# Performance work log

Hardware: AMD Instinct MI355X
Metric: run time of the kernel (lower is better)

## Reference

```python
import jax, jax.numpy as jnp
import numpy as np

HIDDEN = 1024
NUM_HEADS = 16
HEAD_DIM = HIDDEN // NUM_HEADS


def setup_inputs() -> dict:
    key = jax.random.key(0)
    ks = jax.random.split(key, 10)
    B, S = 2, 2048
    inp = {
        "hidden_state": jax.random.normal(ks[0], (B, S, HIDDEN), dtype=jnp.float32),
        "attention_mask": jnp.ones((B, S), dtype=jnp.int32),
        # Linear params (weights stored as [in, out] for x @ W + b)
        "Wq": jax.random.normal(ks[1], (HIDDEN, HIDDEN), dtype=jnp.float32) * 0.02,
        "bq": jnp.zeros((HIDDEN,), dtype=jnp.float32),
        "Wk": jax.random.normal(ks[2], (HIDDEN, HEAD_DIM), dtype=jnp.float32) * 0.02,
        "bk": jnp.zeros((HEAD_DIM,), dtype=jnp.float32),
        "Wv": jax.random.normal(ks[3], (HIDDEN, HEAD_DIM), dtype=jnp.float32) * 0.02,
        "bv": jnp.zeros((HEAD_DIM,), dtype=jnp.float32),
        "Wo": jax.random.normal(ks[4], (HIDDEN, HIDDEN), dtype=jnp.float32) * 0.02,
        "bo": jnp.zeros((HIDDEN,), dtype=jnp.float32),
    }
    return inp


def reference(hidden_state, attention_mask, Wq, bq, Wk, bk, Wv, bv, Wo, bo):
    B, S, H = hidden_state.shape
    nH, hd = NUM_HEADS, HEAD_DIM
    q = hidden_state @ Wq + bq                      # [B,S,H]
    k = hidden_state @ Wk + bk                      # [B,S,hd] (single shared KV head)
    v = hidden_state @ Wv + bv                      # [B,S,hd]
    q = q.reshape(B, S, nH, hd).transpose(0, 2, 1, 3)  # [B,nH,S,hd]
    # scores: broadcast shared K across heads
    scores = jnp.einsum("bhqd,bkd->bhqk", q, k) / jnp.sqrt(jnp.float32(hd))
    mask = (attention_mask[:, None, None, :] != 0)
    scores = jnp.where(mask, scores, jnp.float32(-jnp.inf))
    attn = jax.nn.softmax(scores, axis=-1)          # [B,nH,S,S]
    ctx = jnp.einsum("bhqk,bkd->bhqd", attn, v)     # [B,nH,S,hd]
    ctx = ctx.transpose(0, 2, 1, 3).reshape(B, S, H)
    return ctx @ Wo + bo
```

## Files before the change

kernel.cpp:

```cpp
#include <hip/hip_runtime.h>

#define SEQ   2048
#define NHEAD 16
#define HD    64
#define HID   1024
#define NQKV  1152
#define MROWS 4096

typedef unsigned short u16;
typedef unsigned int u32;
typedef __attribute__((ext_vector_type(8))) __bf16 bfrag;
typedef __attribute__((ext_vector_type(4))) float f32x4;
typedef __attribute__((ext_vector_type(4))) short s16x4;

__device__ __forceinline__ u16 f2bf(float f) {
  unsigned u = __float_as_uint(f);
  u += 0x7fffu + ((u >> 16) & 1u);
  return (u16)(u >> 16);
}

__global__ void k_cvt_x(const float* __restrict__ x, u16* __restrict__ o) {
  int i = (blockIdx.x * 256 + threadIdx.x) * 4;
  float4 v = *reinterpret_cast<const float4*>(x + i);
  s16x4 r;
  r.x = (short)f2bf(v.x); r.y = (short)f2bf(v.y);
  r.z = (short)f2bf(v.z); r.w = (short)f2bf(v.w);
  *reinterpret_cast<s16x4*>(o + i) = r;
}

__global__ void k_tr(const float* __restrict__ src, int ld, u16* __restrict__ dst, int nOff) {
  __shared__ float T[64][65];
  const int t = threadIdx.x;
  const int k0 = blockIdx.x * 64, n0 = blockIdx.y * 64;
#pragma unroll
  for (int p = 0; p < 4; ++p) {
    int r = p * 16 + (t >> 4), c = (t & 15) * 4;
    float4 v = *reinterpret_cast<const float4*>(&src[(size_t)(k0 + r) * ld + n0 + c]);
    T[r][c] = v.x; T[r][c + 1] = v.y; T[r][c + 2] = v.z; T[r][c + 3] = v.w;
  }
  __syncthreads();
#pragma unroll
  for (int p = 0; p < 2; ++p) {
    int cc = t + p * 256;
    int n = cc >> 3, k8 = (cc & 7) * 8;
    union { float4 v; u16 u[8]; } o;
#pragma unroll
    for (int j = 0; j < 8; ++j) o.u[j] = f2bf(T[k8 + j][n]);
    *reinterpret_cast<float4*>(&dst[(size_t)(nOff + n0 + n) * 1024 + k0 + k8]) = o.v;
  }
}

__global__ void k_bias(const float* __restrict__ bq, const float* __restrict__ bk,
                       const float* __restrict__ bv, float* __restrict__ bqkv) {
  int t = blockIdx.x * 256 + threadIdx.x;
  if (t >= NQKV) return;
  float v;
  if (t < 1024)      v = bq[t];
  else if (t < 1088) v = bk[t - 1024];
  else               v = bv[t - 1088];
  bqkv[t] = v;
}

__global__ void k_mb(const int* __restrict__ am, float* __restrict__ Mbias) {
  int t = blockIdx.x * 256 + threadIdx.x;
  if (t < 2 * SEQ) Mbias[t] = am[t] ? 0.0f : -1e30f;
}

__global__ void k_vt(const u16* __restrict__ QKV, u16* __restrict__ Vt) {
  int t = blockIdx.x * 256 + threadIdx.x;
  int s = t & 2047, d = (t >> 11) & 63, b = t >> 17;
  Vt[t] = QKV[(size_t)(b * SEQ + s) * NQKV + 1088 + d];
}

template <int STORE_BF16>
__global__ __launch_bounds__(256) void k_gemm(const u16* __restrict__ A,
                                              const u16* __restrict__ Bt,
                                              const float* __restrict__ bias,
                                              void* __restrict__ Cout,
                                              int M, int N, int K) {
  __shared__ __align__(16) u16 Al[128 * 64];
  __shared__ __align__(16) u16 Bl[64 * 64];
  const int tid = threadIdx.x;
  const int lane = tid & 63, l16 = lane & 15, lg = lane >> 4;
  const int wid = tid >> 6;
  const int m0 = blockIdx.x * 128, n0 = blockIdx.y * 64;
  f32x4 acc[2][4] = {};
  for (int k0 = 0; k0 < K; k0 += 64) {
#pragma unroll
    for (int p = 0; p < 4; ++p) {
      int c = tid + p * 256;
      int r = c >> 3, sl = c & 7;
      __builtin_amdgcn_global_load_lds(
          (__attribute__((address_space(1))) void*)(A + (size_t)(m0 + r) * K + k0 + ((sl ^ (r & 7)) << 3)),
          (__attribute__((address_space(3))) void*)(Al + c * 8), 16, 0, 0);
    }
#pragma unroll
    for (int p = 0; p < 2; ++p) {
      int c = tid + p * 256;
      int r = c >> 3, sl = c & 7;
      __builtin_amdgcn_global_load_lds(
          (__attribute__((address_space(1))) void*)(Bt + (size_t)(n0 + r) * K + k0 + ((sl ^ (r & 7)) << 3)),
          (__attribute__((address_space(3))) void*)(Bl + c * 8), 16, 0, 0);
    }
    __syncthreads();
#pragma unroll
    for (int kk = 0; kk < 2; ++kk) {
      bfrag a[2], b[4];
#pragma unroll
      for (int mi = 0; mi < 2; ++mi) {
        int row = wid * 32 + mi * 16 + l16;
        a[mi] = *reinterpret_cast<const bfrag*>(
            Al + row * 64 + ((((kk << 2) | lg) ^ (l16 & 7)) << 3));
      }
#pragma unroll
      for (int ni = 0; ni < 4; ++ni) {
        int row = ni * 16 + l16;
        b[ni] = *reinterpret_cast<const bfrag*>(
            Bl + row * 64 + ((((kk << 2) | lg) ^ (l16 & 7)) << 3));
      }
#pragma unroll
      for (int mi = 0; mi < 2; ++mi)
#pragma unroll
        for (int ni = 0; ni < 4; ++ni)
          acc[mi][ni] = __builtin_amdgcn_mfma_f32_16x16x32_bf16(a[mi], b[ni], acc[mi][ni], 0, 0, 0);
    }
    __syncthreads();
  }
#pragma unroll
  for (int mi = 0; mi < 2; ++mi)
#pragma unroll
    for (int ni = 0; ni < 4; ++ni) {
      int col = n0 + ni * 16 + l16;
      float bb = bias[col];
#pragma unroll
      for (int r = 0; r < 4; ++r) {
        int row = m0 + wid * 32 + mi * 16 + lg * 4 + r;
        float v = acc[mi][ni][r] + bb;
        if (STORE_BF16) ((u16*)Cout)[(size_t)row * N + col] = f2bf(v);
        else            ((float*)Cout)[(size_t)row * N + col] = v;
      }
    }
}

__global__ __launch_bounds__(256, 4) void k_attn(const u16* __restrict__ QKV,
                                                 const u16* __restrict__ Vt,
                                                 const float* __restrict__ Mbias,
                                                 u16* __restrict__ ctx) {
  __shared__ __align__(16) u16 Kl[2][64 * 64];
  __shared__ __align__(16) u16 Pl[4][16][72];
  const int tid = threadIdx.x;
  const int lane = tid & 63, l16 = lane & 15, lg = lane >> 4, wid = tid >> 6;
  const int q0 = blockIdx.x * 64 + wid * 16;
  const int h = blockIdx.y, b = blockIdx.z;

  const u16* Qrow = QKV + (size_t)(b * SEQ + q0 + l16) * NQKV + h * 64;
  const bfrag aq0 = *reinterpret_cast<const bfrag*>(Qrow + lg * 8);
  const bfrag aq1 = *reinterpret_cast<const bfrag*>(Qrow + 32 + lg * 8);
  const u16* Vb = Vt + (size_t)b * 64 * SEQ;
  const u16* Kg = QKV + (size_t)b * SEQ * NQKV + HID;
  const float* mb = Mbias + b * SEQ;

  auto stage_k = [&](int buf, int kv) {
#pragma unroll
    for (int hh = 0; hh < 2; ++hh) {
      int c = tid + hh * 256;
      int r = c >> 3, cb = (c & 7) ^ (r & 7);
      __builtin_amdgcn_global_load_lds(
          (__attribute__((address_space(1))) void*)(Kg + (size_t)(kv + r) * NQKV + cb * 8),
          (__attribute__((address_space(3))) void*)(&Kl[buf][c * 8]), 16, 0, 0);
    }
  };

  stage_k(0, 0);
  __syncthreads();

  float mrun = -1e30f, lrun = 0.0f;
  f32x4 accO[4] = {};

  for (int it = 0; it < SEQ / 64; ++it) {
    const int kv = it * 64;
    const int cur = it & 1;
    if (it + 1 < SEQ / 64) stage_k(cur ^ 1, kv + 64);

    bfrag vf[4][2];
#pragma unroll
    for (int nt = 0; nt < 4; ++nt)
#pragma unroll
      for (int kb = 0; kb < 2; ++kb)
        vf[nt][kb] = *reinterpret_cast<const bfrag*>(
            Vb + (size_t)(nt * 16 + l16) * SEQ + kv + kb * 32 + lg * 8);

    f32x4 s[4];
#pragma unroll
    for (int nt = 0; nt < 4; ++nt) {
      f32x4 z = {};
      {
        int row = nt * 16 + l16;
        int cb0 = (0 * 4 + lg) ^ (l16 & 7);
        int cb1 = (1 * 4 + lg) ^ (l16 & 7);
        bfrag ak0 = *reinterpret_cast<const bfrag*>(&Kl[cur][row * 64 + cb0 * 8]);
        bfrag ak1 = *reinterpret_cast<const bfrag*>(&Kl[cur][row * 64 + cb1 * 8]);
        z = __builtin_amdgcn_mfma_f32_16x16x32_bf16(ak0, aq0, z, 0, 0, 0);
        z = __builtin_amdgcn_mfma_f32_16x16x32_bf16(ak1, aq1, z, 0, 0, 0);
      }
      s[nt] = z;
    }
#pragma unroll
    for (int nt = 0; nt < 4; ++nt) {
      f32x4 mbv = *reinterpret_cast<const f32x4*>(&mb[kv + nt * 16 + lg * 4]);
#pragma unroll
      for (int r = 0; r < 4; ++r)
        s[nt][r] = s[nt][r] * 0.125f + mbv[r];
    }
    float tmax = s[0][0];
#pragma unroll
    for (int nt = 0; nt < 4; ++nt)
#pragma unroll
      for (int r = 0; r < 4; ++r) tmax = fmaxf(tmax, s[nt][r]);
    tmax = fmaxf(tmax, __shfl_xor(tmax, 16));
    tmax = fmaxf(tmax, __shfl_xor(tmax, 32));
    float mnew = fmaxf(mrun, tmax);
    float alpha = __expf(mrun - mnew);
    mrun = mnew;
    float rsum = 0.0f;
#pragma unroll
    for (int nt = 0; nt < 4; ++nt)
#pragma unroll
      for (int r = 0; r < 4; ++r) {
        s[nt][r] = __expf(s[nt][r] - mnew);
        rsum += s[nt][r];
      }
    rsum += __shfl_xor(rsum, 16);
    rsum += __shfl_xor(rsum, 32);
    lrun = lrun * alpha + rsum;
    float ar[4];
#pragma unroll
    for (int r = 0; r < 4; ++r) ar[r] = __shfl(alpha, lg * 4 + r);
#pragma unroll
    for (int nt = 0; nt < 4; ++nt)
#pragma unroll
      for (int r = 0; r < 4; ++r) accO[nt][r] *= ar[r];
#pragma unroll
    for (int nt = 0; nt < 4; ++nt)
#pragma unroll
      for (int r = 0; r < 4; ++r)
        Pl[wid][l16][nt * 16 + lg * 4 + r] = f2bf(s[nt][r]);
    bfrag ap0 = *reinterpret_cast<const bfrag*>(&Pl[wid][l16][lg * 8]);
    bfrag ap1 = *reinterpret_cast<const bfrag*>(&Pl[wid][l16][32 + lg * 8]);
#pragma unroll
    for (int nt = 0; nt < 4; ++nt) {
      accO[nt] = __builtin_amdgcn_mfma_f32_16x16x32_bf16(ap0, vf[nt][0], accO[nt], 0, 0, 0);
      accO[nt] = __builtin_amdgcn_mfma_f32_16x16x32_bf16(ap1, vf[nt][1], accO[nt], 0, 0, 0);
    }
    __syncthreads();
  }

  float linv = 1.0f / lrun;
  float lr[4];
#pragma unroll
  for (int r = 0; r < 4; ++r) lr[r] = __shfl(linv, lg * 4 + r);
#pragma unroll
  for (int nt = 0; nt < 4; ++nt)
#pragma unroll
    for (int r = 0; r < 4; ++r)
      ctx[(size_t)(b * SEQ + q0 + lg * 4 + r) * HID + h * 64 + nt * 16 + l16] =
          f2bf(accO[nt][r] * lr[r]);
}

extern "C" void kernel_launch(void* const* d_in, const int* in_sizes, int n_in,
                              void* d_out, int out_size, void* d_ws, size_t ws_size,
                              hipStream_t stream) {
  const float* x  = (const float*)d_in[0];
  const int* am   = (const int*)d_in[1];
  const float* Wq = (const float*)d_in[2];
  const float* bq = (const float*)d_in[3];
  const float* Wk = (const float*)d_in[4];
  const float* bk = (const float*)d_in[5];
  const float* Wv = (const float*)d_in[6];
  const float* bv = (const float*)d_in[7];
  const float* Wo = (const float*)d_in[8];
  const float* bo = (const float*)d_in[9];

  char* ws = (char*)d_ws;
  u16*  Xb     = (u16*)(ws + 0);
  u16*  Wt_qkv = (u16*)(ws + 8388608);
  u16*  Wt_o   = (u16*)(ws + 10747904);
  float* bqkv  = (float*)(ws + 12845056);
  float* Mbias = (float*)(ws + 12849664);
  u16*  QKV    = (u16*)(ws + 12866048);
  u16*  Vt     = (u16*)(ws + 22303232);
  u16*  ctx    = (u16*)(ws + 22827520);

  k_cvt_x<<<4096, 256, 0, stream>>>(x, Xb);
  k_tr<<<dim3(16, 16), 256, 0, stream>>>(Wq, 1024, Wt_qkv, 0);
  k_tr<<<dim3(16, 1), 256, 0, stream>>>(Wk, 64, Wt_qkv, 1024);
  k_tr<<<dim3(16, 1), 256, 0, stream>>>(Wv, 64, Wt_qkv, 1088);
  k_tr<<<dim3(16, 16), 256, 0, stream>>>(Wo, 1024, Wt_o, 0);
  k_bias<<<5, 256, 0, stream>>>(bq, bk, bv, bqkv);
  k_mb<<<16, 256, 0, stream>>>(am, Mbias);

  dim3 g1(32, 18);
  k_gemm<1><<<g1, 256, 0, stream>>>(Xb, Wt_qkv, bqkv, (void*)QKV, MROWS, NQKV, HID);

  k_vt<<<1024, 256, 0, stream>>>(QKV, Vt);

  dim3 g2(SEQ / 64, NHEAD, 2);
  k_attn<<<g2, 256, 0, stream>>>(QKV, Vt, Mbias, ctx);

  dim3 g3(32, 16);
  k_gemm<0><<<g3, 256, 0, stream>>>(ctx, Wt_o, bo, d_out, MROWS, HID, HID);
}
```

Before: 278.5 us.

## Rework attention with 32x32 MFMA, lazy rescaling and tiled V transpose

Result: faster. 225.2 us (-19.1%).

```diff
diff --git a/kernel.cpp b/kernel.cpp
--- a/kernel.cpp
+++ b/kernel.cpp
@@ -11,12 +11,19 @@
 typedef unsigned int u32;
 typedef __attribute__((ext_vector_type(8))) __bf16 bfrag;
 typedef __attribute__((ext_vector_type(4))) float f32x4;
+typedef __attribute__((ext_vector_type(16))) float f32x16;
 typedef __attribute__((ext_vector_type(4))) short s16x4;
 
 __device__ __forceinline__ u16 f2bf(float f) {
   unsigned u = __float_as_uint(f);
   u += 0x7fffu + ((u >> 16) & 1u);
   return (u16)(u >> 16);
+}
+
+__device__ __forceinline__ u32 cvtpk_bf16(float lo, float hi) {
+  u32 r;
+  asm("v_cvt_pk_bf16_f32 %0, %1, %2" : "=v"(r) : "v"(lo), "v"(hi));
+  return r;
 }
 
 __global__ void k_cvt_x(const float* __restrict__ x, u16* __restrict__ o) {
@@ -67,9 +74,26 @@
 }
 
 __global__ void k_vt(const u16* __restrict__ QKV, u16* __restrict__ Vt) {
-  int t = blockIdx.x * 256 + threadIdx.x;
-  int s = t & 2047, d = (t >> 11) & 63, b = t >> 17;
-  Vt[t] = QKV[(size_t)(b * SEQ + s) * NQKV + 1088 + d];
+  __shared__ u16 T[64][72];
+  const int t = threadIdx.x;
+  const int s0 = blockIdx.x * 64, b = blockIdx.y;
+#pragma unroll
+  for (int p = 0; p < 2; ++p) {
+    int c = t + p * 256;
+    int r = c >> 3, ch = c & 7;
+    *reinterpret_cast<float4*>(&T[r][ch * 8]) = *reinterpret_cast<const float4*>(
+        &QKV[(size_t)(b * SEQ + s0 + r) * NQKV + 1088 + ch * 8]);
+  }
+  __syncthreads();
+#pragma unroll
+  for (int p = 0; p < 2; ++p) {
+    int cc = t + p * 256;
+    int d = cc >> 3, sc = cc & 7;
+    union { float4 v; u16 u[8]; } o;
+#pragma unroll
+    for (int j = 0; j < 8; ++j) o.u[j] = T[sc * 8 + j][d];
+    *reinterpret_cast<float4*>(&Vt[((size_t)b * 64 + d) * SEQ + s0 + sc * 8]) = o.v;
+  }
 }
 
 template <int STORE_BF16>
@@ -142,28 +166,31 @@
     }
 }
 
-__global__ __launch_bounds__(256, 4) void k_attn(const u16* __restrict__ QKV,
+__global__ __launch_bounds__(128, 2) void k_attn(const u16* __restrict__ QKV,
                                                  const u16* __restrict__ Vt,
                                                  const float* __restrict__ Mbias,
                                                  u16* __restrict__ ctx) {
   __shared__ __align__(16) u16 Kl[2][64 * 64];
-  __shared__ __align__(16) u16 Pl[4][16][72];
+  __shared__ __align__(16) u16 Pl[2][32][72];
   const int tid = threadIdx.x;
-  const int lane = tid & 63, l16 = lane & 15, lg = lane >> 4, wid = tid >> 6;
-  const int q0 = blockIdx.x * 64 + wid * 16;
+  const int lane = tid & 63, l32 = lane & 31, hi = lane >> 5, wid = tid >> 6;
+  const int qw = blockIdx.x * 64 + wid * 32;
   const int h = blockIdx.y, b = blockIdx.z;
 
-  const u16* Qrow = QKV + (size_t)(b * SEQ + q0 + l16) * NQKV + h * 64;
-  const bfrag aq0 = *reinterpret_cast<const bfrag*>(Qrow + lg * 8);
-  const bfrag aq1 = *reinterpret_cast<const bfrag*>(Qrow + 32 + lg * 8);
+  const u16* Qrow = QKV + (size_t)(b * SEQ + qw + l32) * NQKV + h * 64;
+  bfrag Qf[4];
+#pragma unroll
+  for (int ds = 0; ds < 4; ++ds)
+    Qf[ds] = *reinterpret_cast<const bfrag*>(Qrow + ds * 16 + 8 * hi);
+
   const u16* Vb = Vt + (size_t)b * 64 * SEQ;
   const u16* Kg = QKV + (size_t)b * SEQ * NQKV + HID;
   const float* mb = Mbias + b * SEQ;
 
   auto stage_k = [&](int buf, int kv) {
 #pragma unroll
-    for (int hh = 0; hh < 2; ++hh) {
-      int c = tid + hh * 256;
+    for (int hh = 0; hh < 4; ++hh) {
+      int c = tid + hh * 128;
       int r = c >> 3, cb = (c & 7) ^ (r & 7);
       __builtin_amdgcn_global_load_lds(
           (__attribute__((address_space(1))) void*)(Kg + (size_t)(kv + r) * NQKV + cb * 8),
@@ -175,96 +202,101 @@
   __syncthreads();
 
   float mrun = -1e30f, lrun = 0.0f;
-  f32x4 accO[4] = {};
+  f32x16 accO0 = {}, accO1 = {};
 
   for (int it = 0; it < SEQ / 64; ++it) {
-    const int kv = it * 64;
-    const int cur = it & 1;
-    if (it + 1 < SEQ / 64) stage_k(cur ^ 1, kv + 64);
-
-    bfrag vf[4][2];
-#pragma unroll
-    for (int nt = 0; nt < 4; ++nt)
-#pragma unroll
-      for (int kb = 0; kb < 2; ++kb)
-        vf[nt][kb] = *reinterpret_cast<const bfrag*>(
-            Vb + (size_t)(nt * 16 + l16) * SEQ + kv + kb * 32 + lg * 8);
-
-    f32x4 s[4];
-#pragma unroll
-    for (int nt = 0; nt < 4; ++nt) {
-      f32x4 z = {};
-      {
-        int row = nt * 16 + l16;
-        int cb0 = (0 * 4 + lg) ^ (l16 & 7);
-        int cb1 = (1 * 4 + lg) ^ (l16 & 7);
-        bfrag ak0 = *reinterpret_cast<const bfrag*>(&Kl[cur][row * 64 + cb0 * 8]);
-        bfrag ak1 = *reinterpret_cast<const bfrag*>(&Kl[cur][row * 64 + cb1 * 8]);
-        z = __builtin_amdgcn_mfma_f32_16x16x32_bf16(ak0, aq0, z, 0, 0, 0);
-        z = __builtin_amdgcn_mfma_f32_16x16x32_bf16(ak1, aq1, z, 0, 0, 0);
+    const int kv0 = it * 64, cur = it & 1;
+    if (it + 1 < SEQ / 64) stage_k(cur ^ 1, kv0 + 64);
+
+    bfrag Vf0[4];
+#pragma unroll
+    for (int ks = 0; ks < 4; ++ks)
+      Vf0[ks] = *reinterpret_cast<const bfrag*>(
+          Vb + (size_t)l32 * SEQ + kv0 + ks * 16 + 8 * hi);
+
+    f32x16 p0 = {}, p1 = {};
+#pragma unroll
+    for (int ds = 0; ds < 4; ++ds) {
+      const int slot = (2 * ds + hi) ^ (l32 & 7);
+      bfrag k0 = *reinterpret_cast<const bfrag*>(&Kl[cur][l32 * 64 + (slot << 3)]);
+      bfrag k1 = *reinterpret_cast<const bfrag*>(&Kl[cur][(32 + l32) * 64 + (slot << 3)]);
+      p0 = __builtin_amdgcn_mfma_f32_32x32x16_bf16(k0, Qf[ds], p0, 0, 0, 0);
+      p1 = __builtin_amdgcn_mfma_f32_32x32x16_bf16(k1, Qf[ds], p1, 0, 0, 0);
+    }
+
+#pragma unroll
+    for (int rq = 0; rq < 4; ++rq) {
+      f32x4 m0 = *reinterpret_cast<const f32x4*>(&mb[kv0 + 8 * rq + 4 * hi]);
+      f32x4 m1 = *reinterpret_cast<const f32x4*>(&mb[kv0 + 32 + 8 * rq + 4 * hi]);
+#pragma unroll
+      for (int r2 = 0; r2 < 4; ++r2) {
+        p0[rq * 4 + r2] = p0[rq * 4 + r2] * 0.125f + m0[r2];
+        p1[rq * 4 + r2] = p1[rq * 4 + r2] * 0.125f + m1[r2];
       }
-      s[nt] = z;
-    }
-#pragma unroll
-    for (int nt = 0; nt < 4; ++nt) {
-      f32x4 mbv = *reinterpret_cast<const f32x4*>(&mb[kv + nt * 16 + lg * 4]);
-#pragma unroll
-      for (int r = 0; r < 4; ++r)
-        s[nt][r] = s[nt][r] * 0.125f + mbv[r];
-    }
-    float tmax = s[0][0];
-#pragma unroll
-    for (int nt = 0; nt < 4; ++nt)
-#pragma unroll
-      for (int r = 0; r < 4; ++r) tmax = fmaxf(tmax, s[nt][r]);
-    tmax = fmaxf(tmax, __shfl_xor(tmax, 16));
+    }
+
+    float tmax = fmaxf(p0[0], p1[0]);
+#pragma unroll
+    for (int r = 1; r < 16; ++r) tmax = fmaxf(tmax, fmaxf(p0[r], p1[r]));
     tmax = fmaxf(tmax, __shfl_xor(tmax, 32));
-    float mnew = fmaxf(mrun, tmax);
-    float alpha = __expf(mrun - mnew);
-    mrun = mnew;
+
+    if (!__all(tmax - mrun <= 8.0f)) {
+      float mnew = fmaxf(mrun, tmax);
+      float alpha = __expf(mrun - mnew);
+      mrun = mnew;
+      lrun *= alpha;
+#pragma unroll
+      for (int r = 0; r < 16; ++r) { accO0[r] *= alpha; accO1[r] *= alpha; }
+    }
+
     float rsum = 0.0f;
 #pragma unroll
-    for (int nt = 0; nt < 4; ++nt)
-#pragma unroll
-      for (int r = 0; r < 4; ++r) {
-        s[nt][r] = __expf(s[nt][r] - mnew);
-        rsum += s[nt][r];
-      }
-    rsum += __shfl_xor(rsum, 16);
+    for (int r = 0; r < 16; ++r) {
+      p0[r] = __expf(p0[r] - mrun);
+      p1[r] = __expf(p1[r] - mrun);
+      rsum += p0[r] + p1[r];
+    }
     rsum += __shfl_xor(rsum, 32);
-    lrun = lrun * alpha + rsum;
-    float ar[4];
-#pragma unroll
-    for (int r = 0; r < 4; ++r) ar[r] = __shfl(alpha, lg * 4 + r);
-#pragma unroll
-    for (int nt = 0; nt < 4; ++nt)
-#pragma unroll
-      for (int r = 0; r < 4; ++r) accO[nt][r] *= ar[r];
-#pragma unroll
-    for (int nt = 0; nt < 4; ++nt)
-#pragma unroll
-      for (int r = 0; r < 4; ++r)
-        Pl[wid][l16][nt * 16 + lg * 4 + r] = f2bf(s[nt][r]);
-    bfrag ap0 = *reinterpret_cast<const bfrag*>(&Pl[wid][l16][lg * 8]);
-    bfrag ap1 = *reinterpret_cast<const bfrag*>(&Pl[wid][l16][32 + lg * 8]);
-#pragma unroll
-    for (int nt = 0; nt < 4; ++nt) {
-      accO[nt] = __builtin_amdgcn_mfma_f32_16x16x32_bf16(ap0, vf[nt][0], accO[nt], 0, 0, 0);
-      accO[nt] = __builtin_amdgcn_mfma_f32_16x16x32_bf16(ap1, vf[nt][1], accO[nt], 0, 0, 0);
+    lrun += rsum;
+
+#pragma unroll
+    for (int rq = 0; rq < 4; ++rq) {
+      uint2 w0, w1;
+      w0.x = cvtpk_bf16(p0[rq * 4 + 0], p0[rq * 4 + 1]);
+      w0.y = cvtpk_bf16(p0[rq * 4 + 2], p0[rq * 4 + 3]);
+      w1.x = cvtpk_bf16(p1[rq * 4 + 0], p1[rq * 4 + 1]);
+      w1.y = cvtpk_bf16(p1[rq * 4 + 2], p1[rq * 4 + 3]);
+      *reinterpret_cast<uint2*>(&Pl[wid][l32][8 * rq + 4 * hi]) = w0;
+      *reinterpret_cast<uint2*>(&Pl[wid][l32][32 + 8 * rq + 4 * hi]) = w1;
+    }
+
+    bfrag Vf1[4];
+#pragma unroll
+    for (int ks = 0; ks < 4; ++ks)
+      Vf1[ks] = *reinterpret_cast<const bfrag*>(
+          Vb + (size_t)(32 + l32) * SEQ + kv0 + ks * 16 + 8 * hi);
+
+#pragma unroll
+    for (int ks = 0; ks < 4; ++ks) {
+      bfrag Pf = *reinterpret_cast<const bfrag*>(&Pl[wid][l32][ks * 16 + 8 * hi]);
+      accO0 = __builtin_amdgcn_mfma_f32_32x32x16_bf16(Vf0[ks], Pf, accO0, 0, 0, 0);
+      accO1 = __builtin_amdgcn_mfma_f32_32x32x16_bf16(Vf1[ks], Pf, accO1, 0, 0, 0);
     }
     __syncthreads();
   }
 
   float linv = 1.0f / lrun;
-  float lr[4];
-#pragma unroll
-  for (int r = 0; r < 4; ++r) lr[r] = __shfl(linv, lg * 4 + r);
-#pragma unroll
-  for (int nt = 0; nt < 4; ++nt)
-#pragma unroll
-    for (int r = 0; r < 4; ++r)
-      ctx[(size_t)(b * SEQ + q0 + lg * 4 + r) * HID + h * 64 + nt * 16 + l16] =
-          f2bf(accO[nt][r] * lr[r]);
+  size_t base = (size_t)(b * SEQ + qw + l32) * HID + h * 64;
+#pragma unroll
+  for (int rq = 0; rq < 4; ++rq) {
+    uint2 w0, w1;
+    w0.x = cvtpk_bf16(accO0[rq * 4 + 0] * linv, accO0[rq * 4 + 1] * linv);
+    w0.y = cvtpk_bf16(accO0[rq * 4 + 2] * linv, accO0[rq * 4 + 3] * linv);
+    w1.x = cvtpk_bf16(accO1[rq * 4 + 0] * linv, accO1[rq * 4 + 1] * linv);
+    w1.y = cvtpk_bf16(accO1[rq * 4 + 2] * linv, accO1[rq * 4 + 3] * linv);
+    *reinterpret_cast<uint2*>(&ctx[base + 8 * rq + 4 * hi]) = w0;
+    *reinterpret_cast<uint2*>(&ctx[base + 32 + 8 * rq + 4 * hi]) = w1;
+  }
 }
 
 extern "C" void kernel_launch(void* const* d_in, const int* in_sizes, int n_in,
@@ -302,10 +334,10 @@
   dim3 g1(32, 18);
   k_gemm<1><<<g1, 256, 0, stream>>>(Xb, Wt_qkv, bqkv, (void*)QKV, MROWS, NQKV, HID);
 
-  k_vt<<<1024, 256, 0, stream>>>(QKV, Vt);
+  k_vt<<<dim3(32, 2), 256, 0, stream>>>(QKV, Vt);
 
   dim3 g2(SEQ / 64, NHEAD, 2);
-  k_attn<<<g2, 256, 0, stream>>>(QKV, Vt, Mbias, ctx);
+  k_attn<<<g2, 128, 0, stream>>>(QKV, Vt, Mbias, ctx);
 
   dim3 g3(32, 16);
   k_gemm<0><<<g3, 256, 0, stream>>>(ctx, Wt_o, bo, d_out, MROWS, HID, HID);
```
